# Kernel optimization log

Hardware: AMD Instinct MI355X
Metric: run time of the kernel (lower is better)

## Reference

```python
import jax, jax.numpy as jnp
import numpy as np

BATCH = 2048
FEAT = 512
HIDDEN = 512
NUM_CLASSES = 1000


def setup_inputs() -> dict:
    key = jax.random.key(0)
    k1, k2, k3, k4 = jax.random.split(key, 4)
    Z = jax.random.normal(k1, (BATCH, FEAT), dtype=jnp.float32)
    y = jax.random.randint(k2, (BATCH,), 0, NUM_CLASSES)
    W1 = jax.random.normal(k3, (NUM_CLASSES, HIDDEN, FEAT), dtype=jnp.float32)
    b1 = jnp.zeros((NUM_CLASSES, HIDDEN), dtype=jnp.float32)
    W2 = jax.random.normal(k4, (NUM_CLASSES, HIDDEN), dtype=jnp.float32)
    b2 = jnp.zeros((NUM_CLASSES,), dtype=jnp.float32)
    return {"Z": Z, "y": y, "W1": W1, "b1": b1, "W2": W2, "b2": b2}


def reference(Z, y, W1, b1, W2, b2):
    # Per-sample class-indexed weights: w1 [B, H, F], b1 [B, H], w2 [B, H], b2 [B]
    # hidden = tanh(w1 @ Z + b1); out = w2 . hidden + b2
    h = jnp.tanh(jnp.einsum('bhf,bf->bh', W1[y], Z) + b1[y])  # [B, H]
    op = jnp.einsum('bh,bh->b', W2[y], h) + b2[y]             # [B]
    return op
```

## Files before the change

### kernel.cpp

```cpp
#include <hip/hip_runtime.h>
#include <math.h>

#define BATCH 2048
#define FEAT 512
#define HIDDEN 512
#define NUM_CLASSES 1000
#define SCHUNK 8
#define NTHREADS 256
#define QROWS 128
#define NQ 4
#define MAXN 16

#define WS_NACT 0
#define WS_ACT  16
#define WS_CNT  (WS_ACT + NUM_CLASSES)
#define WS_IDX  (WS_CNT + NUM_CLASSES)

__device__ __forceinline__ float fast_tanh(float x) {
    float e = __expf(2.0f * x);
    return 1.0f - 2.0f / (e + 1.0f);
}

__global__ __launch_bounds__(1024) void gather_kernel(const int* __restrict__ y,
                                                      int* __restrict__ ws) {
    __shared__ int s_cnt[NUM_CLASSES];
    const int tid = threadIdx.x;
    if (tid == 0) ws[WS_NACT] = 0;
    if (tid < NUM_CLASSES) s_cnt[tid] = 0;
    __syncthreads();
    #pragma unroll
    for (int i = 0; i < 2; ++i) {
        const int b = tid + i * 1024;
        const int c = y[b];
        const int p = atomicAdd(&s_cnt[c], 1);
        if (p < MAXN) ws[WS_IDX + c * MAXN + p] = b;
    }
    __syncthreads();
    if (tid < NUM_CLASSES) {
        const int cnt = s_cnt[tid];
        ws[WS_CNT + tid] = cnt;
        if (cnt > 0) {
            const int a = atomicAdd(&ws[WS_NACT], 1);
            ws[WS_ACT + a] = tid;
        }
    }
}

__global__ __launch_bounds__(NTHREADS) void disc2l_kernel(
    const float* __restrict__ Z, const int* __restrict__ ws,
    const float* __restrict__ W1, const float* __restrict__ b1,
    const float* __restrict__ W2, const float* __restrict__ b2,
    float* __restrict__ out)
{
    const int a       = blockIdx.x >> 2;
    const int quarter = blockIdx.x & 3;
    if (a >= ws[WS_NACT]) return;

    const int tid  = threadIdx.x;
    const int lane = tid & 63;
    const int wave = tid >> 6;
    const int q    = lane >> 4;
    const int ms   = lane & 15;

    const int c = ws[WS_ACT + a];
    const int n = min(ws[WS_CNT + c], MAXN);

    __shared__ int   s_idx[MAXN];
    __shared__ float s_z[SCHUNK][FEAT];
    __shared__ float s_b1[QROWS];
    __shared__ float s_w2[QROWS];
    __shared__ float s_part[4][SCHUNK];

    if (tid < MAXN) s_idx[tid] = (tid < n) ? ws[WS_IDX + c * MAXN + tid] : 0;

    const int row0 = quarter * QROWS;
    {
        const float4* b1v = (const float4*)(b1 + (size_t)c * HIDDEN + row0);
        const float4* w2v = (const float4*)(W2 + (size_t)c * HIDDEN + row0);
        if (tid < 32)      ((float4*)s_b1)[tid]      = b1v[tid];
        else if (tid < 64) ((float4*)s_w2)[tid - 32] = w2v[tid - 32];
    }
    const float* W1c = W1 + (size_t)c * HIDDEN * FEAT;
    const float  b2c = (quarter == 0) ? b2[c] : 0.0f;

    for (int cb = 0; cb < n; cb += SCHUNK) {
        const int cn = min(SCHUNK, n - cb);

        __syncthreads();
        #pragma unroll
        for (int s0 = 0; s0 < SCHUNK; s0 += 2) {
            const int s = s0 + (tid >> 7);
            if (s < cn) {
                const float4* Zs = (const float4*)(Z + (size_t)s_idx[cb + s] * FEAT);
                ((float4*)s_z[s])[tid & 127] = Zs[tid & 127];
            }
        }
        __syncthreads();

        float oacc = 0.0f;

        for (int g = wave; g < QROWS / 8; g += 4) {
            const int rla = 8 * g + q;
            const int rlb = 8 * g + 4 + q;
            const float4* Wa = (const float4*)(W1c + (size_t)(row0 + rla) * FEAT);
            const float4* Wb = (const float4*)(W1c + (size_t)(row0 + rlb) * FEAT);

            float4 wa[8], wb[8];
            #pragma unroll
            for (int k = 0; k < 8; ++k) {
                wa[k] = Wa[k * 16 + ms];
                wb[k] = Wb[k * 16 + ms];
            }

            float pa[SCHUNK], pb[SCHUNK];
            #pragma unroll
            for (int s = 0; s < SCHUNK; ++s) { pa[s] = 0.0f; pb[s] = 0.0f; }

            #pragma unroll
            for (int k = 0; k < 8; ++k) {
                #pragma unroll
                for (int s = 0; s < SCHUNK; ++s) {
                    if (s < cn) {
                        const float4 zv = ((const float4*)(&s_z[s][k * 64]))[ms];
                        pa[s] += wa[k].x * zv.x + wa[k].y * zv.y
                               + wa[k].z * zv.z + wa[k].w * zv.w;
                        pb[s] += wb[k].x * zv.x + wb[k].y * zv.y
                               + wb[k].z * zv.z + wb[k].w * zv.w;
                    }
                }
            }

            #pragma unroll
            for (int s = 0; s < SCHUNK; ++s) {
                if (s < cn) {
                    pa[s] += __shfl_xor(pa[s], 1, 64);
                    pa[s] += __shfl_xor(pa[s], 2, 64);
                    pa[s] += __shfl_xor(pa[s], 4, 64);
                    pa[s] += __shfl_xor(pa[s], 8, 64);
                    pb[s] += __shfl_xor(pb[s], 1, 64);
                    pb[s] += __shfl_xor(pb[s], 2, 64);
                    pb[s] += __shfl_xor(pb[s], 4, 64);
                    pb[s] += __shfl_xor(pb[s], 8, 64);
                }
            }

            if (ms < cn) {
                float va = pa[0], vb = pb[0];
                #pragma unroll
                for (int s = 1; s < SCHUNK; ++s)
                    if (ms == s) { va = pa[s]; vb = pb[s]; }
                const float ta = fast_tanh(va + s_b1[rla]);
                const float tb = fast_tanh(vb + s_b1[rlb]);
                oacc += s_w2[rla] * ta + s_w2[rlb] * tb;
            }
        }

        oacc += __shfl_xor(oacc, 16, 64);
        oacc += __shfl_xor(oacc, 32, 64);
        if (lane < cn) s_part[wave][lane] = oacc;
        __syncthreads();
        if (tid < cn) {
            float o = b2c;
            #pragma unroll
            for (int w = 0; w < 4; ++w) o += s_part[w][tid];
            atomicAdd(&out[s_idx[cb + tid]], o);
        }
    }
}

extern "C" void kernel_launch(void* const* d_in, const int* in_sizes, int n_in,
                              void* d_out, int out_size, void* d_ws, size_t ws_size,
                              hipStream_t stream) {
    const float* Z  = (const float*)d_in[0];
    const int*   y  = (const int*)d_in[1];
    const float* W1 = (const float*)d_in[2];
    const float* b1 = (const float*)d_in[3];
    const float* W2 = (const float*)d_in[4];
    const float* b2 = (const float*)d_in[5];
    float* out = (float*)d_out;
    int*   ws  = (int*)d_ws;

    (void)hipMemsetAsync(out, 0, (size_t)out_size * sizeof(float), stream);
    gather_kernel<<<1, 1024, 0, stream>>>(y, ws);
    disc2l_kernel<<<NUM_CLASSES * NQ, NTHREADS, 0, stream>>>(Z, ws, W1, b1, W2, b2, out);
}
```

Before: 184.4 us.

## Prefetch W1 rows into registers, pack class descriptors, fold output zeroing into gather

Each disc2l block now loads its first W1 row group into registers before the Z staging and syncs. Inside the row loop it prefetches the next group's W1 rows right after the FMA phase, so global load latency overlaps the shuffle reduction and tanh work. The gather kernel writes a compact per-active-class descriptor (class, count, sample indices), which replaces several dependent workspace lookups and the shared index copy. It also zeroes the output, which removes the separate memset launch. The cost is higher register pressure from keeping prefetched float4 arrays live, plus an extra sync and global pass in the single-block gather kernel.

```diff
diff --git a/kernel.cpp b/kernel.cpp
--- a/kernel.cpp
+++ b/kernel.cpp
@@ -10,11 +10,9 @@
 #define QROWS 128
 #define NQ 4
 #define MAXN 16
-
-#define WS_NACT 0
-#define WS_ACT  16
-#define WS_CNT  (WS_ACT + NUM_CLASSES)
-#define WS_IDX  (WS_CNT + NUM_CLASSES)
+#define DSTRIDE 20
+
+#define WS_TMPIDX (NUM_CLASSES * DSTRIDE)
 
 __device__ __forceinline__ float fast_tanh(float x) {
     float e = __expf(2.0f * x);
@@ -22,26 +20,36 @@
 }
 
 __global__ __launch_bounds__(1024) void gather_kernel(const int* __restrict__ y,
-                                                      int* __restrict__ ws) {
+                                                      int* __restrict__ ws,
+                                                      float* __restrict__ out) {
     __shared__ int s_cnt[NUM_CLASSES];
+    __shared__ int s_nact;
     const int tid = threadIdx.x;
-    if (tid == 0) ws[WS_NACT] = 0;
+    if (tid == 0) s_nact = 0;
     if (tid < NUM_CLASSES) s_cnt[tid] = 0;
+    out[tid] = 0.0f;
+    out[tid + 1024] = 0.0f;
     __syncthreads();
     #pragma unroll
     for (int i = 0; i < 2; ++i) {
         const int b = tid + i * 1024;
-        const int c = y[b];
-        const int p = atomicAdd(&s_cnt[c], 1);
-        if (p < MAXN) ws[WS_IDX + c * MAXN + p] = b;
-    }
+        const int cls = y[b];
+        const int p = atomicAdd(&s_cnt[cls], 1);
+        if (p < MAXN) ws[WS_TMPIDX + cls * MAXN + p] = b;
+    }
+    __syncthreads();
+    if (tid < NUM_CLASSES) ws[tid * DSTRIDE] = -1;
     __syncthreads();
     if (tid < NUM_CLASSES) {
         const int cnt = s_cnt[tid];
-        ws[WS_CNT + tid] = cnt;
         if (cnt > 0) {
-            const int a = atomicAdd(&ws[WS_NACT], 1);
-            ws[WS_ACT + a] = tid;
+            const int a = atomicAdd(&s_nact, 1);
+            int* d = ws + a * DSTRIDE;
+            d[0] = tid;
+            d[1] = min(cnt, MAXN);
+            #pragma unroll
+            for (int k = 0; k < MAXN; ++k)
+                d[4 + k] = (k < cnt) ? ws[WS_TMPIDX + tid * MAXN + k] : 0;
         }
     }
 }
@@ -54,45 +62,54 @@
 {
     const int a       = blockIdx.x >> 2;
     const int quarter = blockIdx.x & 3;
-    if (a >= ws[WS_NACT]) return;
-
     const int tid  = threadIdx.x;
     const int lane = tid & 63;
     const int wave = tid >> 6;
     const int q    = lane >> 4;
     const int ms   = lane & 15;
 
-    const int c = ws[WS_ACT + a];
-    const int n = min(ws[WS_CNT + c], MAXN);
-
-    __shared__ int   s_idx[MAXN];
+    const int* __restrict__ desc = ws + a * DSTRIDE;
+    const int c = desc[0];
+    if (c < 0) return;
+    const int n = desc[1];
+
     __shared__ float s_z[SCHUNK][FEAT];
     __shared__ float s_b1[QROWS];
     __shared__ float s_w2[QROWS];
     __shared__ float s_part[4][SCHUNK];
 
-    if (tid < MAXN) s_idx[tid] = (tid < n) ? ws[WS_IDX + c * MAXN + tid] : 0;
-
     const int row0 = quarter * QROWS;
+    const float* W1c = W1 + (size_t)c * HIDDEN * FEAT + (size_t)row0 * FEAT;
+
+    float4 wa[8], wb[8];
     {
-        const float4* b1v = (const float4*)(b1 + (size_t)c * HIDDEN + row0);
-        const float4* w2v = (const float4*)(W2 + (size_t)c * HIDDEN + row0);
-        if (tid < 32)      ((float4*)s_b1)[tid]      = b1v[tid];
-        else if (tid < 64) ((float4*)s_w2)[tid - 32] = w2v[tid - 32];
-    }
-    const float* W1c = W1 + (size_t)c * HIDDEN * FEAT;
-    const float  b2c = (quarter == 0) ? b2[c] : 0.0f;
+        const float4* Wa = (const float4*)(W1c + (size_t)(8 * wave + q) * FEAT);
+        const float4* Wb = (const float4*)(W1c + (size_t)(8 * wave + 4 + q) * FEAT);
+        #pragma unroll
+        for (int k = 0; k < 8; ++k) { wa[k] = Wa[k * 16 + ms]; wb[k] = Wb[k * 16 + ms]; }
+    }
+
+    if (tid < 32)      ((float4*)s_b1)[tid]      = ((const float4*)(b1 + (size_t)c * HIDDEN + row0))[tid];
+    else if (tid < 64) ((float4*)s_w2)[tid - 32] = ((const float4*)(W2 + (size_t)c * HIDDEN + row0))[tid - 32];
+
+    const float b2c = (quarter == 0) ? b2[c] : 0.0f;
 
     for (int cb = 0; cb < n; cb += SCHUNK) {
         const int cn = min(SCHUNK, n - cb);
 
-        __syncthreads();
+        if (cb > 0) {
+            const float4* Wa = (const float4*)(W1c + (size_t)(8 * wave + q) * FEAT);
+            const float4* Wb = (const float4*)(W1c + (size_t)(8 * wave + 4 + q) * FEAT);
+            #pragma unroll
+            for (int k = 0; k < 8; ++k) { wa[k] = Wa[k * 16 + ms]; wb[k] = Wb[k * 16 + ms]; }
+        }
+
         #pragma unroll
         for (int s0 = 0; s0 < SCHUNK; s0 += 2) {
             const int s = s0 + (tid >> 7);
             if (s < cn) {
-                const float4* Zs = (const float4*)(Z + (size_t)s_idx[cb + s] * FEAT);
-                ((float4*)s_z[s])[tid & 127] = Zs[tid & 127];
+                const int zi = desc[4 + cb + s];
+                ((float4*)s_z[s])[tid & 127] = ((const float4*)(Z + (size_t)zi * FEAT))[tid & 127];
             }
         }
         __syncthreads();
@@ -102,15 +119,6 @@
         for (int g = wave; g < QROWS / 8; g += 4) {
             const int rla = 8 * g + q;
             const int rlb = 8 * g + 4 + q;
-            const float4* Wa = (const float4*)(W1c + (size_t)(row0 + rla) * FEAT);
-            const float4* Wb = (const float4*)(W1c + (size_t)(row0 + rlb) * FEAT);
-
-            float4 wa[8], wb[8];
-            #pragma unroll
-            for (int k = 0; k < 8; ++k) {
-                wa[k] = Wa[k * 16 + ms];
-                wb[k] = Wb[k * 16 + ms];
-            }
 
             float pa[SCHUNK], pb[SCHUNK];
             #pragma unroll
@@ -130,6 +138,13 @@
                 }
             }
 
+            if (g + 4 < QROWS / 8) {
+                const float4* Wa = (const float4*)(W1c + (size_t)(8 * (g + 4) + q) * FEAT);
+                const float4* Wb = (const float4*)(W1c + (size_t)(8 * (g + 4) + 4 + q) * FEAT);
+                #pragma unroll
+                for (int k = 0; k < 8; ++k) { wa[k] = Wa[k * 16 + ms]; wb[k] = Wb[k * 16 + ms]; }
+            }
+
             #pragma unroll
             for (int s = 0; s < SCHUNK; ++s) {
                 if (s < cn) {
@@ -163,7 +178,7 @@
             float o = b2c;
             #pragma unroll
             for (int w = 0; w < 4; ++w) o += s_part[w][tid];
-            atomicAdd(&out[s_idx[cb + tid]], o);
+            atomicAdd(&out[desc[4 + cb + tid]], o);
         }
     }
 }
@@ -180,7 +195,6 @@
     float* out = (float*)d_out;
     int*   ws  = (int*)d_ws;
 
-    (void)hipMemsetAsync(out, 0, (size_t)out_size * sizeof(float), stream);
-    gather_kernel<<<1, 1024, 0, stream>>>(y, ws);
+    gather_kernel<<<1, 1024, 0, stream>>>(y, ws, out);
     disc2l_kernel<<<NUM_CLASSES * NQ, NTHREADS, 0, stream>>>(Z, ws, W1, b1, W2, b2, out);
 }
```

Result: no change. 185.7 us (+0.7%).
